# Optimization experiments

Hardware: AMD Instinct MI355X
Metric: run time of the kernel (lower is better)

The kernel has to match this reference:

```python
import jax, jax.numpy as jnp
import numpy as np

NUM_NODES = 200000  # num_user + num_item
DIM_E = 64
NUM_EDGES = 600000
EPS = 1e-12
NEG_SLOPE = 0.01  # F.leaky_relu default


def setup_inputs() -> dict:
    key = jax.random.key(0)
    k1, k2, k3 = jax.random.split(key, 3)
    # xavier_normal on [N, D]: std = sqrt(2/(fan_in+fan_out))
    std = float(np.sqrt(2.0 / (NUM_NODES + DIM_E)))
    id_embedding = jax.random.normal(k1, (NUM_NODES, DIM_E), dtype=jnp.float32) * std
    edge_index = jax.random.randint(k2, (2, NUM_EDGES), 0, NUM_NODES, dtype=jnp.int64)
    weight_vector = jax.random.uniform(k3, (2 * NUM_EDGES, 1), dtype=jnp.float32)
    return {"id_embedding": id_embedding, "edge_index": edge_index,
            "weight_vector": weight_vector}


def _l2_normalize(x):
    # F.normalize(x, p=2, dim=1, eps=1e-12)
    n = jnp.sqrt(jnp.sum(x * x, axis=1, keepdims=True))
    return x / jnp.maximum(n, EPS)


def _leaky_relu(x):
    return jnp.where(x >= 0, x, NEG_SLOPE * x)


def reference(id_embedding, edge_index, weight_vector):
    N = id_embedding.shape[0]
    # symmetrize: cat(edge_index, edge_index[[1,0]])
    ei = jnp.concatenate([edge_index, edge_index[::-1]], axis=1)
    src, dst = ei[0], ei[1]  # messages flow src -> dst (PyG source_to_target)
    cnt = jax.ops.segment_sum(jnp.ones((src.shape[0],), jnp.float32), dst,
                              num_segments=N)[:, None]
    denom = jnp.maximum(cnt, 1.0)  # isolated nodes: sum is 0, mean defined as 0

    def conv(x):
        msg = x[src] * weight_vector            # gather + per-edge scale [2E, D]
        agg = jax.ops.segment_sum(msg, dst, num_segments=N)  # scatter-sum [N, D]
        return agg / denom                      # scatter-mean

    x = _l2_normalize(id_embedding)
    x1 = _leaky_relu(conv(x))
    x2 = _leaky_relu(conv(x1))
    return x + x1 + x2
```

## Files before the change

### kernel.cpp

```cpp
#include <hip/hip_runtime.h>
#include <hip/hip_fp16.h>

#define DIM 64
#define NEG_SLOPE 0.01f
#define BKT 512
#define TILE 2048

typedef unsigned u32;
typedef unsigned long long u64;


__global__ void k_norm_hist(const float* __restrict__ emb,
                            __half* __restrict__ x0h,
                            const int* __restrict__ p,
                            u32* __restrict__ mat,
                            int N, int E, int rb, int B, int nblkE) {
    if ((int)blockIdx.x < rb) {
        int lane = threadIdx.x & 63;
        int row  = blockIdx.x * 16 + (threadIdx.x >> 6) * 4 + (lane >> 4);
        int l16  = lane & 15;
        if (row >= N) return;
        float4 v = *(const float4*)(emb + (size_t)row * DIM + l16 * 4);
        float s = v.x * v.x + v.y * v.y + v.z * v.z + v.w * v.w;
        #pragma unroll
        for (int m = 1; m < 16; m <<= 1) s += __shfl_xor(s, m, 64);
        float inv = 1.0f / fmaxf(sqrtf(s), 1e-12f);
        union { uint2 u; __half2 h[2]; } pk;
        pk.h[0] = __floats2half2_rn(v.x * inv, v.y * inv);
        pk.h[1] = __floats2half2_rn(v.z * inv, v.w * inv);
        *(uint2*)(x0h + (size_t)row * DIM + l16 * 4) = pk.u;
    } else {
        __shared__ u32 hist[BKT];
        int blk = blockIdx.x - rb;
        int t = threadIdx.x;
        for (int i = t; i < B; i += 256) hist[i] = 0;
        __syncthreads();
        int base = blk * TILE;
        #pragma unroll
        for (int k = 0; k < TILE / 256; k++) {
            int e = base + k * 256 + t;
            if (e < 2 * E) {
                int dst = (e < E) ? p[e + E] : p[e - E];
                atomicAdd(&hist[(u32)dst >> 9], 1u);
            }
        }
        __syncthreads();
        for (int i = t; i < B; i += 256) mat[(size_t)i * nblkE + blk] = hist[i];
    }
}

__global__ void k_scan1(const u32* __restrict__ in, u32* __restrict__ out,
                        u32* __restrict__ bsum, int M) {
    __shared__ u32 sdata[256];
    int t = threadIdx.x;
    int base = blockIdx.x * TILE + t * 8;
    u32 v[8]; u32 tsum = 0;
    #pragma unroll
    for (int k = 0; k < 8; k++) {
        int i = base + k;
        v[k] = (i < M) ? in[i] : 0u;
        tsum += v[k];
    }
    sdata[t] = tsum;
    __syncthreads();
    for (int off = 1; off < 256; off <<= 1) {
        u32 x = (t >= off) ? sdata[t - off] : 0u;
        __syncthreads();
        sdata[t] += x;
        __syncthreads();
    }
    u32 run = sdata[t] - tsum;
    if (t == 255) bsum[blockIdx.x] = sdata[255];
    #pragma unroll
    for (int k = 0; k < 8; k++) {
        int i = base + k;
        if (i < M) out[i] = run;
        run += v[k];
    }
}

__global__ void k_scan2(u32* __restrict__ bsum, int nb) {
    __shared__ u32 sdata[256];
    int t = threadIdx.x;
    u32 v = (t < nb) ? bsum[t] : 0u;
    sdata[t] = v;
    __syncthreads();
    for (int off = 1; off < 256; off <<= 1) {
        u32 x = (t >= off) ? sdata[t - off] : 0u;
        __syncthreads();
        sdata[t] += x;
        __syncthreads();
    }
    if (t < nb) bsum[t] = sdata[t] - v;
}

__global__ void k_scanfix(u32* __restrict__ mscan,
                          const u32* __restrict__ bsum, int M) {
    int i = blockIdx.x * 256 + threadIdx.x;
    if (i >= M) return;
    mscan[i] += bsum[i >> 11];
}

__global__ void k_place(const int* __restrict__ p, const float* __restrict__ w,
                        const u32* __restrict__ mscan,
                        u64* __restrict__ places, int E, int nblkE) {
    __shared__ u32 cur[BKT];
    int blk = blockIdx.x;
    int t = threadIdx.x;
    for (int i = t; i < BKT; i += 256) cur[i] = 0;
    __syncthreads();
    int base = blk * TILE;
    #pragma unroll
    for (int k = 0; k < TILE / 256; k++) {
        int e = base + k * 256 + t;
        if (e >= 2 * E) continue;
        int src = p[e];
        int dst = (e < E) ? p[e + E] : p[e - E];
        u32 bin = (u32)dst >> 9;
        u32 w14 = (u32)(w[e] * 16384.0f + 0.5f);
        if (w14 > 16383u) w14 = 16383u;
        u32 rank = atomicAdd(&cur[bin], 1u);
        u32 slot = mscan[(size_t)bin * nblkE + blk] + rank;
        places[slot] = ((u64)((u32)dst & (BKT - 1)) << 32) |
                       (((u32)src << 14) | w14);
    }
}

__global__ void k_bucket(const u64* __restrict__ places,
                         const u32* __restrict__ mscan,
                         u32* __restrict__ row_ptr,
                         u32* __restrict__ colw,
                         int N, int E, int B, int nblkE) {
    __shared__ u32 hist[BKT];
    __shared__ u32 excl[BKT];
    __shared__ u32 sdata[256];
    int b = blockIdx.x;
    int t = threadIdx.x;
    int node0 = b * BKT;
    int nnodes = N - node0; if (nnodes > BKT) nnodes = BKT;
    size_t flat0 = (size_t)b * nblkE;
    u32 seg_s = mscan[flat0];
    u32 seg_e = (b + 1 < B) ? mscan[flat0 + nblkE] : (u32)(2 * E);
    for (int i = t; i < BKT; i += 256) hist[i] = 0;
    __syncthreads();
    for (u32 j = seg_s + t; j < seg_e; j += 256) {
        u64 pl = places[j];
        atomicAdd(&hist[(u32)(pl >> 32)], 1u);
    }
    __syncthreads();
    u32 a0 = hist[2 * t], a1 = hist[2 * t + 1];
    u32 tsum = a0 + a1;
    sdata[t] = tsum;
    __syncthreads();
    for (int off = 1; off < 256; off <<= 1) {
        u32 x = (t >= off) ? sdata[t - off] : 0u;
        __syncthreads();
        sdata[t] += x;
        __syncthreads();
    }
    u32 texcl = sdata[t] - tsum;
    excl[2 * t] = texcl;
    excl[2 * t + 1] = texcl + a0;
    __syncthreads();
    for (int i = t; i < nnodes; i += 256)
        row_ptr[node0 + i] = seg_s + excl[i];
    if (b == 0 && t == 0) row_ptr[N] = (u32)(2 * E);
    __syncthreads();
    for (u32 j = seg_s + t; j < seg_e; j += 256) {
        u64 pl = places[j];
        u32 loc = atomicAdd(&excl[(u32)(pl >> 32)], 1u);
        colw[seg_s + loc] = (u32)pl;
    }
}


__device__ __forceinline__ void gather8(const __half* __restrict__ x,
                                        const u32* __restrict__ colw,
                                        u32 s, u32 e, int g, int sub,
                                        float acc[8]) {
    for (u32 base = s; base < e; base += 8) {
        u32 u = 0;
        if (base + (u32)sub < e) u = colw[base + sub];
        int   cx = (int)(u >> 14);
        float cy = (float)(u & 16383u) * (1.0f / 16384.0f);
        #pragma unroll
        for (int j = 0; j < 8; j++) {
            int   sj = __shfl(cx, (g << 3) | j, 64);
            float wj = __shfl(cy, (g << 3) | j, 64);
            uint4 q = *(const uint4*)(x + (size_t)sj * DIM + sub * 8);
            const __half2* hp = (const __half2*)&q;
            #pragma unroll
            for (int k = 0; k < 4; k++) {
                float2 f = __half22float2(hp[k]);
                acc[2 * k]     += f.x * wj;
                acc[2 * k + 1] += f.y * wj;
            }
        }
    }
}

__global__ void k_conv1(const __half* __restrict__ x0h,
                        const u32* __restrict__ row_ptr,
                        const u32* __restrict__ colw,
                        __half* __restrict__ x1h, int N) {
    int wave = (blockIdx.x * 256 + threadIdx.x) >> 6;
    int g    = (threadIdx.x >> 3) & 7;
    int sub  = threadIdx.x & 7;
    int row  = wave * 8 + g;
    if (row >= N) return;
    u32 s = row_ptr[row], e = row_ptr[row + 1];
    float acc[8] = {0, 0, 0, 0, 0, 0, 0, 0};
    gather8(x0h, colw, s, e, g, sub, acc);
    float rdeno = 1.0f / fmaxf((float)(e - s), 1.0f);
    __half2 hv[4];
    #pragma unroll
    for (int k = 0; k < 4; k++) {
        float v0 = acc[2 * k] * rdeno;
        float v1 = acc[2 * k + 1] * rdeno;
        v0 = (v0 >= 0.0f) ? v0 : NEG_SLOPE * v0;
        v1 = (v1 >= 0.0f) ? v1 : NEG_SLOPE * v1;
        hv[k] = __floats2half2_rn(v0, v1);
    }
    *(uint4*)(x1h + (size_t)row * DIM + sub * 8) = *(const uint4*)hv;
}

__global__ void k_conv2(const __half* __restrict__ x0h,
                        const __half* __restrict__ x1h,
                        const u32* __restrict__ row_ptr,
                        const u32* __restrict__ colw,
                        float* __restrict__ out, int N) {
    int wave = (blockIdx.x * 256 + threadIdx.x) >> 6;
    int g    = (threadIdx.x >> 3) & 7;
    int sub  = threadIdx.x & 7;
    int row  = wave * 8 + g;
    if (row >= N) return;
    u32 s = row_ptr[row], e = row_ptr[row + 1];
    float acc[8] = {0, 0, 0, 0, 0, 0, 0, 0};
    gather8(x1h, colw, s, e, g, sub, acc);
    float rdeno = 1.0f / fmaxf((float)(e - s), 1.0f);
    uint4 q0 = *(const uint4*)(x0h + (size_t)row * DIM + sub * 8);
    uint4 q1 = *(const uint4*)(x1h + (size_t)row * DIM + sub * 8);
    const __half2* h0 = (const __half2*)&q0;
    const __half2* h1 = (const __half2*)&q1;
    float r[8];
    #pragma unroll
    for (int k = 0; k < 4; k++) {
        float2 a = __half22float2(h0[k]);
        float2 b = __half22float2(h1[k]);
        float x2a = acc[2 * k] * rdeno;
        float x2b = acc[2 * k + 1] * rdeno;
        x2a = (x2a >= 0.0f) ? x2a : NEG_SLOPE * x2a;
        x2b = (x2b >= 0.0f) ? x2b : NEG_SLOPE * x2b;
        r[2 * k]     = a.x + b.x + x2a;
        r[2 * k + 1] = a.y + b.y + x2b;
    }
    float* op = out + (size_t)row * DIM + sub * 8;
    *(float4*)(op)     = make_float4(r[0], r[1], r[2], r[3]);
    *(float4*)(op + 4) = make_float4(r[4], r[5], r[6], r[7]);
}

static inline size_t align16(size_t x) { return (x + 15) & ~(size_t)15; }

extern "C" void kernel_launch(void* const* d_in, const int* in_sizes, int n_in,
                              void* d_out, int out_size, void* d_ws, size_t ws_size,
                              hipStream_t stream) {
    const int N = in_sizes[0] / DIM;
    const int E = in_sizes[1] / 2;

    const float* emb = (const float*)d_in[0];
    const int*   ei  = (const int*)d_in[1];
    const float* w   = (const float*)d_in[2];
    float*       out = (float*)d_out;

    const int B     = (N + BKT - 1) / BKT;
    const int nblkE = (2 * E + TILE - 1) / TILE;
    const int M     = B * nblkE;
    const int nb1   = (M + TILE - 1) / TILE;
    const int rb    = (N + 15) / 16;
    const int cvb   = (N + 31) / 32;

    char* ws = (char*)d_ws;
    size_t off = 0;
    __half* x0h    = (__half*)(ws + off); off += align16((size_t)N * DIM * 2);
    __half* x1h    = (__half*)(ws + off); off += align16((size_t)N * DIM * 2);
    u64*    places = (u64*)(ws + off);    off += align16((size_t)2 * E * 8);
    u32*    colw   = (u32*)(ws + off);    off += align16((size_t)2 * E * 4);
    u32*    mat    = (u32*)(ws + off);    off += align16((size_t)M * 4);
    u32*    mscan  = (u32*)(ws + off);    off += align16((size_t)M * 4);
    u32*    row_ptr= (u32*)(ws + off);    off += align16((size_t)(N + 1) * 4);
    u32*    bsum   = (u32*)(ws + off);    off += align16(256 * 4);

    k_norm_hist<<<rb + nblkE, 256, 0, stream>>>(emb, x0h, ei, mat, N, E, rb, B, nblkE);
    k_scan1<<<nb1, 256, 0, stream>>>(mat, mscan, bsum, M);
    k_scan2<<<1, 256, 0, stream>>>(bsum, nb1);
    k_scanfix<<<(M + 255) / 256, 256, 0, stream>>>(mscan, bsum, M);
    k_place<<<nblkE, 256, 0, stream>>>(ei, w, mscan, places, E, nblkE);
    k_bucket<<<B, 256, 0, stream>>>(places, mscan, row_ptr, colw, N, E, B, nblkE);

    k_conv1<<<cvb, 256, 0, stream>>>(x0h, row_ptr, colw, x1h, N);
    k_conv2<<<cvb, 256, 0, stream>>>(x0h, x1h, row_ptr, colw, out, N);
}
```

Baseline: 227.4 us.

## Build CSR with global per-node degree atomics instead of two-level bucket sort

Replaces the bucketed counting sort (per-tile histograms, place into buckets, per-bucket local sort) with a direct CSR build. A global per-node degree histogram is built with atomics, scanned into row_ptr, and each edge is then placed with a global atomicAdd on a per-node cursor. This removes the intermediate 64-bit places buffer and the k_bucket pass. In exchange it relies on many scattered global atomics, and edge order within a row becomes nondeterministic. That can change floating-point summation order, though the sum stays correct.

Measured after the change: 293.2 us. 1.29x slower.

```diff
diff --git a/kernel.cpp b/kernel.cpp
--- a/kernel.cpp
+++ b/kernel.cpp
@@ -3,18 +3,26 @@
 
 #define DIM 64
 #define NEG_SLOPE 0.01f
-#define BKT 512
 #define TILE 2048
 
 typedef unsigned u32;
 typedef unsigned long long u64;
 
 
-__global__ void k_norm_hist(const float* __restrict__ emb,
-                            __half* __restrict__ x0h,
-                            const int* __restrict__ p,
-                            u32* __restrict__ mat,
-                            int N, int E, int rb, int B, int nblkE) {
+__global__ void k_zero(u32* __restrict__ deg, int N) {
+    int i = (blockIdx.x * 256 + threadIdx.x) * 4;
+    if (i + 3 < N) {
+        *(uint4*)(deg + i) = make_uint4(0u, 0u, 0u, 0u);
+    } else {
+        for (int k = i; k < N; k++) deg[k] = 0u;
+    }
+}
+
+__global__ void k_norm_deg(const float* __restrict__ emb,
+                           __half* __restrict__ x0h,
+                           const int* __restrict__ p,
+                           u32* __restrict__ deg,
+                           int N, int E, int rb) {
     if ((int)blockIdx.x < rb) {
         int lane = threadIdx.x & 63;
         int row  = blockIdx.x * 16 + (threadIdx.x >> 6) * 4 + (lane >> 4);
@@ -30,22 +38,16 @@
         pk.h[1] = __floats2half2_rn(v.z * inv, v.w * inv);
         *(uint2*)(x0h + (size_t)row * DIM + l16 * 4) = pk.u;
     } else {
-        __shared__ u32 hist[BKT];
-        int blk = blockIdx.x - rb;
-        int t = threadIdx.x;
-        for (int i = t; i < B; i += 256) hist[i] = 0;
-        __syncthreads();
-        int base = blk * TILE;
-        #pragma unroll
-        for (int k = 0; k < TILE / 256; k++) {
-            int e = base + k * 256 + t;
-            if (e < 2 * E) {
-                int dst = (e < E) ? p[e + E] : p[e - E];
-                atomicAdd(&hist[(u32)dst >> 9], 1u);
-            }
+        int i = ((blockIdx.x - rb) * 256 + threadIdx.x) * 4;
+        if (i + 3 < 2 * E) {
+            int4 v = *(const int4*)(p + i);
+            atomicAdd(&deg[(u32)v.x], 1u);
+            atomicAdd(&deg[(u32)v.y], 1u);
+            atomicAdd(&deg[(u32)v.z], 1u);
+            atomicAdd(&deg[(u32)v.w], 1u);
+        } else {
+            for (int k = i; k < 2 * E; k++) atomicAdd(&deg[(u32)p[k]], 1u);
         }
-        __syncthreads();
-        for (int i = t; i < B; i += 256) mat[(size_t)i * nblkE + blk] = hist[i];
     }
 }
 
@@ -94,83 +96,28 @@
     if (t < nb) bsum[t] = sdata[t] - v;
 }
 
-__global__ void k_scanfix(u32* __restrict__ mscan,
-                          const u32* __restrict__ bsum, int M) {
+__global__ void k_scanfix(const u32* __restrict__ mscan,
+                          const u32* __restrict__ bsum,
+                          u32* __restrict__ row_ptr,
+                          u32* __restrict__ cur, int N, int E2) {
     int i = blockIdx.x * 256 + threadIdx.x;
-    if (i >= M) return;
-    mscan[i] += bsum[i >> 11];
-}
-
-__global__ void k_place(const int* __restrict__ p, const float* __restrict__ w,
-                        const u32* __restrict__ mscan,
-                        u64* __restrict__ places, int E, int nblkE) {
-    __shared__ u32 cur[BKT];
-    int blk = blockIdx.x;
-    int t = threadIdx.x;
-    for (int i = t; i < BKT; i += 256) cur[i] = 0;
-    __syncthreads();
-    int base = blk * TILE;
-    #pragma unroll
-    for (int k = 0; k < TILE / 256; k++) {
-        int e = base + k * 256 + t;
-        if (e >= 2 * E) continue;
-        int src = p[e];
-        int dst = (e < E) ? p[e + E] : p[e - E];
-        u32 bin = (u32)dst >> 9;
-        u32 w14 = (u32)(w[e] * 16384.0f + 0.5f);
-        if (w14 > 16383u) w14 = 16383u;
-        u32 rank = atomicAdd(&cur[bin], 1u);
-        u32 slot = mscan[(size_t)bin * nblkE + blk] + rank;
-        places[slot] = ((u64)((u32)dst & (BKT - 1)) << 32) |
-                       (((u32)src << 14) | w14);
-    }
-}
-
-__global__ void k_bucket(const u64* __restrict__ places,
-                         const u32* __restrict__ mscan,
-                         u32* __restrict__ row_ptr,
-                         u32* __restrict__ colw,
-                         int N, int E, int B, int nblkE) {
-    __shared__ u32 hist[BKT];
-    __shared__ u32 excl[BKT];
-    __shared__ u32 sdata[256];
-    int b = blockIdx.x;
-    int t = threadIdx.x;
-    int node0 = b * BKT;
-    int nnodes = N - node0; if (nnodes > BKT) nnodes = BKT;
-    size_t flat0 = (size_t)b * nblkE;
-    u32 seg_s = mscan[flat0];
-    u32 seg_e = (b + 1 < B) ? mscan[flat0 + nblkE] : (u32)(2 * E);
-    for (int i = t; i < BKT; i += 256) hist[i] = 0;
-    __syncthreads();
-    for (u32 j = seg_s + t; j < seg_e; j += 256) {
-        u64 pl = places[j];
-        atomicAdd(&hist[(u32)(pl >> 32)], 1u);
-    }
-    __syncthreads();
-    u32 a0 = hist[2 * t], a1 = hist[2 * t + 1];
-    u32 tsum = a0 + a1;
-    sdata[t] = tsum;
-    __syncthreads();
-    for (int off = 1; off < 256; off <<= 1) {
-        u32 x = (t >= off) ? sdata[t - off] : 0u;
-        __syncthreads();
-        sdata[t] += x;
-        __syncthreads();
-    }
-    u32 texcl = sdata[t] - tsum;
-    excl[2 * t] = texcl;
-    excl[2 * t + 1] = texcl + a0;
-    __syncthreads();
-    for (int i = t; i < nnodes; i += 256)
-        row_ptr[node0 + i] = seg_s + excl[i];
-    if (b == 0 && t == 0) row_ptr[N] = (u32)(2 * E);
-    __syncthreads();
-    for (u32 j = seg_s + t; j < seg_e; j += 256) {
-        u64 pl = places[j];
-        u32 loc = atomicAdd(&excl[(u32)(pl >> 32)], 1u);
-        colw[seg_s + loc] = (u32)pl;
-    }
+    if (i == 0) row_ptr[N] = (u32)E2;
+    if (i >= N) return;
+    u32 v = mscan[i] + bsum[i >> 11];
+    row_ptr[i] = v;
+    cur[i] = v;
+}
+
+__global__ void k_place2(const int* __restrict__ p, const float* __restrict__ w,
+                         u32* __restrict__ cur, u32* __restrict__ colw, int E) {
+    int e = blockIdx.x * 256 + threadIdx.x;
+    if (e >= 2 * E) return;
+    int src = p[e];
+    int dst = (e < E) ? p[e + E] : p[e - E];
+    u32 w14 = (u32)(w[e] * 16384.0f + 0.5f);
+    if (w14 > 16383u) w14 = 16383u;
+    u32 slot = atomicAdd(&cur[dst], 1u);
+    colw[slot] = ((u32)src << 14) | w14;
 }
 
 
@@ -272,30 +219,30 @@
     const float* w   = (const float*)d_in[2];
     float*       out = (float*)d_out;
 
-    const int B     = (N + BKT - 1) / BKT;
-    const int nblkE = (2 * E + TILE - 1) / TILE;
-    const int M     = B * nblkE;
-    const int nb1   = (M + TILE - 1) / TILE;
-    const int rb    = (N + 15) / 16;
-    const int cvb   = (N + 31) / 32;
+    const int rb   = (N + 15) / 16;
+    const int degb = (2 * E + 1023) / 1024;
+    const int nb1  = (N + TILE - 1) / TILE;
+    const int zb   = (N + 1023) / 1024;
+    const int pb   = (2 * E + 255) / 256;
+    const int cvb  = (N + 31) / 32;
 
     char* ws = (char*)d_ws;
     size_t off = 0;
     __half* x0h    = (__half*)(ws + off); off += align16((size_t)N * DIM * 2);
     __half* x1h    = (__half*)(ws + off); off += align16((size_t)N * DIM * 2);
-    u64*    places = (u64*)(ws + off);    off += align16((size_t)2 * E * 8);
     u32*    colw   = (u32*)(ws + off);    off += align16((size_t)2 * E * 4);
-    u32*    mat    = (u32*)(ws + off);    off += align16((size_t)M * 4);
-    u32*    mscan  = (u32*)(ws + off);    off += align16((size_t)M * 4);
+    u32*    deg    = (u32*)(ws + off);    off += align16((size_t)N * 4);
+    u32*    mscan  = (u32*)(ws + off);    off += align16((size_t)N * 4);
     u32*    row_ptr= (u32*)(ws + off);    off += align16((size_t)(N + 1) * 4);
+    u32*    cur    = (u32*)(ws + off);    off += align16((size_t)N * 4);
     u32*    bsum   = (u32*)(ws + off);    off += align16(256 * 4);
 
-    k_norm_hist<<<rb + nblkE, 256, 0, stream>>>(emb, x0h, ei, mat, N, E, rb, B, nblkE);
-    k_scan1<<<nb1, 256, 0, stream>>>(mat, mscan, bsum, M);
-    k_scan2<<<1, 256, 0, stream>>>(bsum, nb1);
-    k_scanfix<<<(M + 255) / 256, 256, 0, stream>>>(mscan, bsum, M);
-    k_place<<<nblkE, 256, 0, stream>>>(ei, w, mscan, places, E, nblkE);
-    k_bucket<<<B, 256, 0, stream>>>(places, mscan, row_ptr, colw, N, E, B, nblkE);
+    k_zero    <<<zb, 256, 0, stream>>>(deg, N);
+    k_norm_deg<<<rb + degb, 256, 0, stream>>>(emb, x0h, ei, deg, N, E, rb);
+    k_scan1   <<<nb1, 256, 0, stream>>>(deg, mscan, bsum, N);
+    k_scan2   <<<1, 256, 0, stream>>>(bsum, nb1);
+    k_scanfix <<<(N + 255) / 256, 256, 0, stream>>>(mscan, bsum, row_ptr, cur, N, 2 * E);
+    k_place2  <<<pb, 256, 0, stream>>>(ei, w, cur, colw, E);
 
     k_conv1<<<cvb, 256, 0, stream>>>(x0h, row_ptr, colw, x1h, N);
     k_conv2<<<cvb, 256, 0, stream>>>(x0h, x1h, row_ptr, colw, out, N);
```

## Shrink CSR build buckets, split placement payload, fuse scan kernels

Applied to the files above, without the earlier changes.

Halves the destination bucket width so the local node index fits in a byte, and splits the 8-byte placement records into a 4-byte payload array plus a 1-byte local index array. The goal is less memory traffic in the place and bucket passes. The second-level scan is merged into the fix-up kernel, where every block redundantly rescans the block sums, which removes one launch. The gather loop now runs only over valid neighbours instead of a fully unrolled 8, which skips wasted loads on short rows but gives up unrolling. B grows to about 782 buckets, so the shared histograms become fixed 800-entry arrays, which only works while N stays at or below 204800.

New measurement: 250.3 us. 1.1x slower.

```diff
diff --git a/kernel.cpp b/kernel.cpp
--- a/kernel.cpp
+++ b/kernel.cpp
@@ -3,7 +3,7 @@
 
 #define DIM 64
 #define NEG_SLOPE 0.01f
-#define BKT 512
+#define BKT 256
 #define TILE 2048
 
 typedef unsigned u32;
@@ -30,7 +30,7 @@
         pk.h[1] = __floats2half2_rn(v.z * inv, v.w * inv);
         *(uint2*)(x0h + (size_t)row * DIM + l16 * 4) = pk.u;
     } else {
-        __shared__ u32 hist[BKT];
+        __shared__ u32 hist[800];
         int blk = blockIdx.x - rb;
         int t = threadIdx.x;
         for (int i = t; i < B; i += 256) hist[i] = 0;
@@ -41,7 +41,7 @@
             int e = base + k * 256 + t;
             if (e < 2 * E) {
                 int dst = (e < E) ? p[e + E] : p[e - E];
-                atomicAdd(&hist[(u32)dst >> 9], 1u);
+                atomicAdd(&hist[(u32)dst >> 8], 1u);
             }
         }
         __syncthreads();
@@ -79,8 +79,10 @@
     }
 }
 
-__global__ void k_scan2(u32* __restrict__ bsum, int nb) {
+__global__ void k_scanfix(u32* __restrict__ mscan,
+                          const u32* __restrict__ bsum, int nb, int M) {
     __shared__ u32 sdata[256];
+    __shared__ u32 sexcl[256];
     int t = threadIdx.x;
     u32 v = (t < nb) ? bsum[t] : 0u;
     sdata[t] = v;
@@ -91,23 +93,20 @@
         sdata[t] += x;
         __syncthreads();
     }
-    if (t < nb) bsum[t] = sdata[t] - v;
-}
-
-__global__ void k_scanfix(u32* __restrict__ mscan,
-                          const u32* __restrict__ bsum, int M) {
-    int i = blockIdx.x * 256 + threadIdx.x;
-    if (i >= M) return;
-    mscan[i] += bsum[i >> 11];
+    sexcl[t] = sdata[t] - v;
+    __syncthreads();
+    int i = blockIdx.x * 256 + t;
+    if (i < M) mscan[i] += sexcl[i >> 11];
 }
 
 __global__ void k_place(const int* __restrict__ p, const float* __restrict__ w,
                         const u32* __restrict__ mscan,
-                        u64* __restrict__ places, int E, int nblkE) {
-    __shared__ u32 cur[BKT];
+                        u32* __restrict__ pay, unsigned char* __restrict__ loc8,
+                        int E, int nblkE, int B) {
+    __shared__ u32 cur[800];
     int blk = blockIdx.x;
     int t = threadIdx.x;
-    for (int i = t; i < BKT; i += 256) cur[i] = 0;
+    for (int i = t; i < B; i += 256) cur[i] = 0;
     __syncthreads();
     int base = blk * TILE;
     #pragma unroll
@@ -116,17 +115,18 @@
         if (e >= 2 * E) continue;
         int src = p[e];
         int dst = (e < E) ? p[e + E] : p[e - E];
-        u32 bin = (u32)dst >> 9;
+        u32 bin = (u32)dst >> 8;
         u32 w14 = (u32)(w[e] * 16384.0f + 0.5f);
         if (w14 > 16383u) w14 = 16383u;
         u32 rank = atomicAdd(&cur[bin], 1u);
         u32 slot = mscan[(size_t)bin * nblkE + blk] + rank;
-        places[slot] = ((u64)((u32)dst & (BKT - 1)) << 32) |
-                       (((u32)src << 14) | w14);
-    }
-}
-
-__global__ void k_bucket(const u64* __restrict__ places,
+        pay[slot]  = ((u32)src << 14) | w14;
+        loc8[slot] = (unsigned char)((u32)dst & (BKT - 1));
+    }
+}
+
+__global__ void k_bucket(const u32* __restrict__ pay,
+                         const unsigned char* __restrict__ loc8,
                          const u32* __restrict__ mscan,
                          u32* __restrict__ row_ptr,
                          u32* __restrict__ colw,
@@ -141,15 +141,12 @@
     size_t flat0 = (size_t)b * nblkE;
     u32 seg_s = mscan[flat0];
     u32 seg_e = (b + 1 < B) ? mscan[flat0 + nblkE] : (u32)(2 * E);
-    for (int i = t; i < BKT; i += 256) hist[i] = 0;
-    __syncthreads();
-    for (u32 j = seg_s + t; j < seg_e; j += 256) {
-        u64 pl = places[j];
-        atomicAdd(&hist[(u32)(pl >> 32)], 1u);
-    }
-    __syncthreads();
-    u32 a0 = hist[2 * t], a1 = hist[2 * t + 1];
-    u32 tsum = a0 + a1;
+    hist[t] = 0;
+    __syncthreads();
+    for (u32 j = seg_s + t; j < seg_e; j += 256)
+        atomicAdd(&hist[loc8[j]], 1u);
+    __syncthreads();
+    u32 tsum = hist[t];
     sdata[t] = tsum;
     __syncthreads();
     for (int off = 1; off < 256; off <<= 1) {
@@ -159,17 +156,14 @@
         __syncthreads();
     }
     u32 texcl = sdata[t] - tsum;
-    excl[2 * t] = texcl;
-    excl[2 * t + 1] = texcl + a0;
-    __syncthreads();
-    for (int i = t; i < nnodes; i += 256)
-        row_ptr[node0 + i] = seg_s + excl[i];
+    excl[t] = texcl;
+    if (t < nnodes) row_ptr[node0 + t] = seg_s + texcl;
     if (b == 0 && t == 0) row_ptr[N] = (u32)(2 * E);
     __syncthreads();
     for (u32 j = seg_s + t; j < seg_e; j += 256) {
-        u64 pl = places[j];
-        u32 loc = atomicAdd(&excl[(u32)(pl >> 32)], 1u);
-        colw[seg_s + loc] = (u32)pl;
+        u32 loc = loc8[j];
+        u32 pos = atomicAdd(&excl[loc], 1u);
+        colw[seg_s + pos] = pay[j];
     }
 }
 
@@ -179,12 +173,12 @@
                                         u32 s, u32 e, int g, int sub,
                                         float acc[8]) {
     for (u32 base = s; base < e; base += 8) {
+        int m = (int)(e - base); if (m > 8) m = 8;
         u32 u = 0;
-        if (base + (u32)sub < e) u = colw[base + sub];
+        if (sub < m) u = colw[base + sub];
         int   cx = (int)(u >> 14);
         float cy = (float)(u & 16383u) * (1.0f / 16384.0f);
-        #pragma unroll
-        for (int j = 0; j < 8; j++) {
+        for (int j = 0; j < m; j++) {
             int   sj = __shfl(cx, (g << 3) | j, 64);
             float wj = __shfl(cy, (g << 3) | j, 64);
             uint4 q = *(const uint4*)(x + (size_t)sj * DIM + sub * 8);
@@ -281,21 +275,21 @@
 
     char* ws = (char*)d_ws;
     size_t off = 0;
-    __half* x0h    = (__half*)(ws + off); off += align16((size_t)N * DIM * 2);
-    __half* x1h    = (__half*)(ws + off); off += align16((size_t)N * DIM * 2);
-    u64*    places = (u64*)(ws + off);    off += align16((size_t)2 * E * 8);
-    u32*    colw   = (u32*)(ws + off);    off += align16((size_t)2 * E * 4);
-    u32*    mat    = (u32*)(ws + off);    off += align16((size_t)M * 4);
-    u32*    mscan  = (u32*)(ws + off);    off += align16((size_t)M * 4);
-    u32*    row_ptr= (u32*)(ws + off);    off += align16((size_t)(N + 1) * 4);
-    u32*    bsum   = (u32*)(ws + off);    off += align16(256 * 4);
+    __half*        x0h    = (__half*)(ws + off);        off += align16((size_t)N * DIM * 2);
+    __half*        x1h    = (__half*)(ws + off);        off += align16((size_t)N * DIM * 2);
+    u32*           pay    = (u32*)(ws + off);           off += align16((size_t)2 * E * 4);
+    unsigned char* loc8   = (unsigned char*)(ws + off); off += align16((size_t)2 * E);
+    u32*           colw   = (u32*)(ws + off);           off += align16((size_t)2 * E * 4);
+    u32*           mat    = (u32*)(ws + off);           off += align16((size_t)M * 4);
+    u32*           mscan  = (u32*)(ws + off);           off += align16((size_t)M * 4);
+    u32*           row_ptr= (u32*)(ws + off);           off += align16((size_t)(N + 1) * 4);
+    u32*           bsum   = (u32*)(ws + off);           off += align16(256 * 4);
 
     k_norm_hist<<<rb + nblkE, 256, 0, stream>>>(emb, x0h, ei, mat, N, E, rb, B, nblkE);
-    k_scan1<<<nb1, 256, 0, stream>>>(mat, mscan, bsum, M);
-    k_scan2<<<1, 256, 0, stream>>>(bsum, nb1);
-    k_scanfix<<<(M + 255) / 256, 256, 0, stream>>>(mscan, bsum, M);
-    k_place<<<nblkE, 256, 0, stream>>>(ei, w, mscan, places, E, nblkE);
-    k_bucket<<<B, 256, 0, stream>>>(places, mscan, row_ptr, colw, N, E, B, nblkE);
+    k_scan1  <<<nb1, 256, 0, stream>>>(mat, mscan, bsum, M);
+    k_scanfix<<<(M + 255) / 256, 256, 0, stream>>>(mscan, bsum, nb1, M);
+    k_place  <<<nblkE, 256, 0, stream>>>(ei, w, mscan, pay, loc8, E, nblkE, B);
+    k_bucket <<<B, 256, 0, stream>>>(pay, loc8, mscan, row_ptr, colw, N, E, B, nblkE);
 
     k_conv1<<<cvb, 256, 0, stream>>>(x0h, row_ptr, colw, x1h, N);
     k_conv2<<<cvb, 256, 0, stream>>>(x0h, x1h, row_ptr, colw, out, N);
```
